# Kernel tuning notes

Hardware: AMD Instinct MI355X
Metric: run time of the kernel (lower is better)

The kernel has to match this reference:

```python
import jax, jax.numpy as jnp
import numpy as np

WS = 8          # window_size
NH = 8          # num_heads
VD = 512        # values_dim
CD = 128        # coords_dim
INNER = 512     # inner_ratio * values_dim
E = INNER // NH # head_dim = 64
B, Hh, Ww_ = 2, 224, 224

# relative position indices (static)
_idx = np.array([[x, y] for x in range(WS) for y in range(WS)])
_rel = _idx[None, :, :] - _idx[:, None, :] + WS - 1  # (WS^2, WS^2, 2)
REL0 = jnp.asarray(_rel[:, :, 0])
REL1 = jnp.asarray(_rel[:, :, 1])

# shifted-window masks (static)
_s = WS * (WS // 2)
_rm = np.zeros((WS * WS, WS * WS), np.float32)
_rm[-_s:, :-_s] = -np.inf
_rm[:-_s, -_s:] = -np.inf
_cm = _rm.reshape(WS, WS, WS, WS).transpose(1, 0, 3, 2).reshape(WS * WS, WS * WS)
ROW_MASK = jnp.asarray(_rm)
COL_MASK = jnp.asarray(_cm)


def _rmsnorm(x, g, eps=1e-6):
    return x * g * jax.lax.rsqrt(jnp.mean(x * x, axis=-1, keepdims=True) + eps)


def _to_windows(x, b, Wh, Ww):
    # x: (b, hp, wp, INNER) with channel layout (e H) (head fastest)
    x = x.reshape(b, Wh, WS, Ww, WS, E, NH)
    return x.transpose(0, 6, 1, 3, 2, 4, 5).reshape(b, NH, Wh, Ww, WS * WS, E)


def setup_inputs() -> dict:
    key = jax.random.key(0)
    ks = jax.random.split(key, 8)
    s = 0.02
    return {
        "embedded_values": jax.random.normal(ks[0], (B, Hh, Ww_, VD), jnp.float32),
        "embedded_coords": jax.random.normal(ks[1], (B, Hh, Ww_, CD), jnp.float32),
        "Wqk_v": jax.random.normal(ks[2], (VD, 2 * INNER), jnp.float32) * s,
        "bqk_v": jnp.zeros((2 * INNER,), jnp.float32),
        "g_v": jnp.ones((2 * INNER,), jnp.float32),
        "Wv": jax.random.normal(ks[3], (VD, INNER), jnp.float32) * s,
        "bv": jnp.zeros((INNER,), jnp.float32),
        "Wqk_c": jax.random.normal(ks[4], (CD, 2 * INNER), jnp.float32) * s,
        "bqk_c": jnp.zeros((2 * INNER,), jnp.float32),
        "g_c": jnp.ones((2 * INNER,), jnp.float32),
        "pos_emb": jax.random.normal(ks[5], (2 * WS - 1, 2 * WS - 1), jnp.float32),
        "Wout": jax.random.normal(ks[6], (INNER, VD), jnp.float32) * s,
        "bout": jnp.zeros((VD,), jnp.float32),
    }


def reference(embedded_values, embedded_coords, Wqk_v, bqk_v, g_v, Wv, bv,
              Wqk_c, bqk_c, g_c, pos_emb, Wout, bout):
    b, h, w, _ = embedded_values.shape
    # projections; torch concat then rearrange '(d k)' k=3 interleaves channels -> reshape (..., INNER, 3)
    vqk = _rmsnorm(embedded_values @ Wqk_v + bqk_v, g_v)          # (b,h,w,2*INNER)
    vval = embedded_values @ Wv + bv                               # (b,h,w,INNER)
    v = jnp.concatenate([vqk, vval], axis=-1).reshape(b, h, w, INNER, 3)
    c = _rmsnorm(embedded_coords @ Wqk_c + bqk_c, g_c).reshape(b, h, w, INNER, 2)

    pad_h = (-h) % WS
    pad_w = (-w) % WS
    v = jnp.pad(v, ((0, 0), (0, pad_h), (0, pad_w), (0, 0), (0, 0)))
    c = jnp.pad(c, ((0, 0), (0, pad_h), (0, pad_w), (0, 0), (0, 0)))
    # shifted=True: roll windows by half window (no inverse roll in original)
    v = jnp.roll(v, (-(WS // 2), -(WS // 2)), axis=(1, 2))
    c = jnp.roll(c, (-(WS // 2), -(WS // 2)), axis=(1, 2))

    hp, wp = h + pad_h, w + pad_w
    Wh, Ww = hp // WS, wp // WS
    qv = _to_windows(v[..., 0], b, Wh, Ww)
    kv = _to_windows(v[..., 1], b, Wh, Ww)
    vv = _to_windows(v[..., 2], b, Wh, Ww)
    qc = _to_windows(c[..., 0], b, Wh, Ww)
    kc = _to_windows(c[..., 1], b, Wh, Ww)

    scale = float(E) ** 0.5
    dots = (jnp.einsum('bhijpe,bhijqe->bhijpq', qv, kv)
            + jnp.einsum('bhijpe,bhijqe->bhijpq', qc, kc)) / scale
    dots = dots + pos_emb[REL0, REL1]
    # shifted-window masks on last window row / column
    dots = dots.at[:, :, -1, :].add(ROW_MASK)
    dots = dots.at[:, :, :, -1].add(COL_MASK)

    attn = jax.nn.softmax(dots, axis=-1)
    y = jnp.einsum('bhijpq,bhijqe->bhijpe', attn, vv)
    # un-window; output channel layout is (H e) (head slow)
    y = y.reshape(b, NH, Wh, Ww, WS, WS, E).transpose(0, 2, 4, 3, 5, 1, 6)
    y = y.reshape(b, hp, wp, INNER)[:, :h, :w, :]
    return y @ Wout + bout
```

## Files before the change

### kernel.cpp

```cpp
#include <hip/hip_runtime.h>


using u16 = unsigned short;
typedef short bf16x8 __attribute__((ext_vector_type(8)));
typedef float f32x4 __attribute__((ext_vector_type(4)));
typedef u16 u16x4 __attribute__((ext_vector_type(4)));
typedef u16 u16x8 __attribute__((ext_vector_type(8)));

__device__ __forceinline__ float bf2f(u16 v) {
  return __uint_as_float(((unsigned)v) << 16);
}
__device__ __forceinline__ u16 f2bf(float f) {
  unsigned u = __float_as_uint(f);
  u += 0x7fffu + ((u >> 16) & 1u);
  return (u16)(u >> 16);
}

__global__ void prep_wv(const float* __restrict__ Wqkv, const float* __restrict__ Wv,
                        u16* __restrict__ out) {
  int idx = blockIdx.x * 256 + threadIdx.x;
  if (idx >= 1536 * 512) return;
  int j = idx >> 9, kk = idx & 511;
  int t = j >> 9, rr = j & 511, nn = rr >> 6, e = rr & 63;
  int cc = 3 * (e * 8 + nn) + t;
  float v = (cc < 1024) ? Wqkv[kk * 1024 + cc] : Wv[kk * 512 + (cc - 1024)];
  out[idx] = f2bf(v);
}

__global__ void prep_wc(const float* __restrict__ W, u16* __restrict__ out) {
  int idx = blockIdx.x * 256 + threadIdx.x;
  if (idx >= 1024 * 128) return;
  int j = idx >> 7, kk = idx & 127;
  int t = j >> 9, rr = j & 511, nn = rr >> 6, e = rr & 63;
  int cc = 2 * (e * 8 + nn) + t;
  out[idx] = f2bf(W[kk * 1024 + cc]);
}

__global__ void prep_wout(const float* __restrict__ W, u16* __restrict__ out) {
  int idx = blockIdx.x * 256 + threadIdx.x;
  if (idx >= 512 * 512) return;
  int o = idx >> 9, kk = idx & 511;
  out[idx] = f2bf(W[kk * 512 + o]);
}

__global__ void prep_vec(const float* __restrict__ bqkv, const float* __restrict__ g_v,
                         const float* __restrict__ bv, const float* __restrict__ bqkc,
                         const float* __restrict__ g_c,
                         float* __restrict__ bpv, float* __restrict__ gAv, float* __restrict__ gBv,
                         float* __restrict__ bpc, float* __restrict__ gAc, float* __restrict__ gBc) {
  int j = blockIdx.x * 256 + threadIdx.x;
  if (j < 1536) {
    int t = j >> 9, rr = j & 511, nn = rr >> 6, e = rr & 63;
    int cc = 3 * (e * 8 + nn) + t;
    if (cc < 1024) { bpv[j] = bqkv[cc]; gAv[j] = g_v[cc]; gBv[j] = 0.f; }
    else           { bpv[j] = bv[cc - 1024]; gAv[j] = 0.f; gBv[j] = 1.f; }
  }
  if (j < 1024) {
    int t = j >> 9, rr = j & 511, nn = rr >> 6, e = rr & 63;
    int cc = 2 * (e * 8 + nn) + t;
    bpc[j] = bqkc[cc]; gAc[j] = g_c[cc]; gBc[j] = 0.f;
  }
}

__global__ void prep_biasT(const float* __restrict__ pe, float* __restrict__ bT) {
  int idx = blockIdx.x * 256 + threadIdx.x;
  if (idx >= 4 * 4096) return;
  int v = idx >> 12, q = (idx >> 6) & 63, p = idx & 63;
  int ap = p >> 3, bp = p & 7, aq = q >> 3, bq = q & 7;
  float val = pe[(aq - ap + 7) * 15 + (bq - bp + 7)];
  if ((v & 1) && ((ap >= 4) != (aq >= 4))) val = -1e30f;
  if ((v & 2) && ((bp >= 4) != (bq >= 4))) val = -1e30f;
  bT[idx] = val;
}

template<bool AFP32>
__device__ __forceinline__ u16x8 load_conv(const void* base, size_t elemoff) {
  if constexpr (AFP32) {
    const float* p = (const float*)base + elemoff;
    float4 lo = *(const float4*)p;
    float4 hi = *(const float4*)(p + 4);
    u16x8 o;
    o[0] = f2bf(lo.x); o[1] = f2bf(lo.y); o[2] = f2bf(lo.z); o[3] = f2bf(lo.w);
    o[4] = f2bf(hi.x); o[5] = f2bf(hi.y); o[6] = f2bf(hi.z); o[7] = f2bf(hi.w);
    return o;
  } else {
    return *(const u16x8*)((const u16*)base + elemoff);
  }
}

template<int N, int K, int MODE, bool AFP32>
__global__ __launch_bounds__(256) void gemm_bt(
    const void* __restrict__ A, const u16* __restrict__ Bt,
    const float* __restrict__ bias, void* __restrict__ outp,
    float* __restrict__ part, const float* __restrict__ gB) {
  constexpr int NCB = N / 128;
  const int bn = blockIdx.x, bm = blockIdx.y;
  const int tid = threadIdx.x;
  const int wid = tid >> 6;
  const int wr = wid >> 1, wc = wid & 1;
  const int lane = tid & 63;
  const int g = lane >> 4, c = lane & 15;
  const int r0 = tid >> 3, ch = tid & 7;

  __shared__ u16 At[128 * 72];
  __shared__ u16 Bs[128 * 72];

  f32x4 acc[4][4] = {};

  const size_t abase = (size_t)bm * 128 * K;
  const u16* Bg = Bt + (size_t)bn * 128 * K;

  u16x8 areg[4], breg[4];
#pragma unroll
  for (int i = 0; i < 4; ++i) {
    int r = i * 32 + r0;
    areg[i] = load_conv<AFP32>(A, abase + (size_t)r * K + ch * 8);
    breg[i] = *(const u16x8*)(Bg + (size_t)r * K + ch * 8);
  }
  constexpr int KT = K / 64;
  for (int kt = 0; kt < KT; ++kt) {
#pragma unroll
    for (int i = 0; i < 4; ++i) {
      int r = i * 32 + r0;
      *(u16x8*)(At + r * 72 + ch * 8) = areg[i];
      *(u16x8*)(Bs + r * 72 + ch * 8) = breg[i];
    }
    __syncthreads();
    if (kt + 1 < KT) {
      const int k0 = (kt + 1) * 64;
#pragma unroll
      for (int i = 0; i < 4; ++i) {
        int r = i * 32 + r0;
        areg[i] = load_conv<AFP32>(A, abase + (size_t)r * K + k0 + ch * 8);
        breg[i] = *(const u16x8*)(Bg + (size_t)r * K + k0 + ch * 8);
      }
    }
#pragma unroll
    for (int kk = 0; kk < 2; ++kk) {
      bf16x8 af[4], bfv[4];
#pragma unroll
      for (int mi = 0; mi < 4; ++mi)
        af[mi] = *(const bf16x8*)(At + (wr * 64 + mi * 16 + c) * 72 + kk * 32 + g * 8);
#pragma unroll
      for (int ni = 0; ni < 4; ++ni)
        bfv[ni] = *(const bf16x8*)(Bs + (wc * 64 + ni * 16 + c) * 72 + kk * 32 + g * 8);
#pragma unroll
      for (int mi = 0; mi < 4; ++mi)
#pragma unroll
        for (int ni = 0; ni < 4; ++ni)
          acc[mi][ni] = __builtin_amdgcn_mfma_f32_16x16x32_bf16(af[mi], bfv[ni], acc[mi][ni], 0, 0, 0);
    }
    __syncthreads();
  }

  const int rowbase = bm * 128 + wr * 64;
  const int colbase = bn * 128 + wc * 64;
  if constexpr (MODE == 0) {
    u16* O = (u16*)outp;
    float rowsq[4][4];
#pragma unroll
    for (int mi = 0; mi < 4; ++mi)
#pragma unroll
      for (int r = 0; r < 4; ++r) rowsq[mi][r] = 0.f;
#pragma unroll
    for (int ni = 0; ni < 4; ++ni) {
      const int col = colbase + ni * 16 + c;
      const float bb = bias[col];
      const float fl = (gB[col] == 0.f) ? 1.f : 0.f;
#pragma unroll
      for (int mi = 0; mi < 4; ++mi)
#pragma unroll
        for (int r = 0; r < 4; ++r) {
          float v = acc[mi][ni][r] + bb;
          O[(size_t)(rowbase + mi * 16 + g * 4 + r) * N + col] = f2bf(v);
          rowsq[mi][r] += fl * v * v;
        }
    }
#pragma unroll
    for (int mi = 0; mi < 4; ++mi)
#pragma unroll
      for (int r = 0; r < 4; ++r) {
        float s = rowsq[mi][r];
        s += __shfl_xor(s, 1); s += __shfl_xor(s, 2);
        s += __shfl_xor(s, 4); s += __shfl_xor(s, 8);
        rowsq[mi][r] = s;
      }
    __syncthreads();
    float* red = (float*)At;
    if (c == 0) {
#pragma unroll
      for (int mi = 0; mi < 4; ++mi)
#pragma unroll
        for (int r = 0; r < 4; ++r)
          red[wc * 128 + wr * 64 + mi * 16 + g * 4 + r] = rowsq[mi][r];
    }
    __syncthreads();
    if (tid < 128)
      part[(size_t)(bm * 128 + tid) * NCB + bn] = red[tid] + red[128 + tid];
  } else {
    float* O = (float*)outp;
#pragma unroll
    for (int ni = 0; ni < 4; ++ni) {
      const int col = colbase + ni * 16 + c;
      const float bb = bias[col];
#pragma unroll
      for (int mi = 0; mi < 4; ++mi)
#pragma unroll
        for (int r = 0; r < 4; ++r)
          O[(size_t)(rowbase + mi * 16 + g * 4 + r) * N + col] = acc[mi][ni][r] + bb;
    }
  }
}

__global__ void combine_scales(const float* __restrict__ pvp, const float* __restrict__ pcp,
                               float* __restrict__ sv, float* __restrict__ sc) {
  const int i = blockIdx.x * 256 + threadIdx.x;
  float s = 0.f;
#pragma unroll
  for (int k = 0; k < 12; ++k) s += pvp[(size_t)i * 12 + k];
  sv[i] = rsqrtf(s * (1.f / 1024.f) + 1e-6f);
  float s2 = 0.f;
#pragma unroll
  for (int k = 0; k < 8; ++k) s2 += pcp[(size_t)i * 8 + k];
  sc[i] = rsqrtf(s2 * (1.f / 1024.f) + 1e-6f);
}

__device__ __forceinline__ void store_norm(u16* dst, u16x8 raw, const float* gA,
                                           const float* gB, float s, int e0) {
  u16x8 o;
#pragma unroll
  for (int j = 0; j < 8; ++j) {
    float fac = gA[e0 + j] * s + gB[e0 + j];
    o[j] = f2bf(bf2f(raw[j]) * fac);
  }
  *(u16x8*)dst = o;
}

__global__ __launch_bounds__(64) void attn_kernel(
    const u16* __restrict__ Pv, const u16* __restrict__ Pc,
    const float* __restrict__ sv, const float* __restrict__ sc,
    const float* __restrict__ gAv, const float* __restrict__ gBv,
    const float* __restrict__ gAc, const float* __restrict__ gBc,
    const float* __restrict__ biasT, u16* __restrict__ Y) {
  const int l = threadIdx.x;
  int bx = blockIdx.x;
  const int wj = bx % 28; bx /= 28;
  const int wi = bx % 28; bx /= 28;
  const int n = bx & 7;
  const int bi = bx >> 3;

  const int g = l >> 4, c = l & 15;
  const int rr0 = l >> 3, rch = l & 7;

  __shared__ u16 Ka[64 * 72];
  __shared__ u16 Qa[64 * 72];
  __shared__ float gf[640];

  gf[l]       = gAv[n * 64 + l];          gf[64 + l]  = gBv[n * 64 + l];
  gf[128 + l] = gAv[512 + n * 64 + l];    gf[192 + l] = gBv[512 + n * 64 + l];
  gf[256 + l] = gAv[1024 + n * 64 + l];   gf[320 + l] = gBv[1024 + n * 64 + l];
  gf[384 + l] = gAc[n * 64 + l];          gf[448 + l] = gBc[n * 64 + l];
  gf[512 + l] = gAc[512 + n * 64 + l];    gf[576 + l] = gBc[512 + n * 64 + l];

  auto pixof = [&](int a, int b2) -> int {
    int y = wi * 8 + a + 4; if (y >= 224) y -= 224;
    int x = wj * 8 + b2 + 4; if (x >= 224) x -= 224;
    return (bi * 224 + y) * 224 + x;
  };

#pragma unroll
  for (int i = 0; i < 8; ++i) {
    const int pix = pixof(i, rr0);
    const float s = sv[pix];
    const u16* src = Pv + (size_t)pix * 1536 + n * 64 + rch * 8;
    u16x8 q = *(const u16x8*)src;
    u16x8 k = *(const u16x8*)(src + 512);
    store_norm(Qa + (i * 8 + rr0) * 72 + rch * 8, q, gf, gf + 64, s, rch * 8);
    store_norm(Ka + (i * 8 + rr0) * 72 + rch * 8, k, gf + 128, gf + 192, s, rch * 8);
  }

  f32x4 acc[4][4] = {};
  auto qk_accum = [&]() {
#pragma unroll
    for (int kk = 0; kk < 2; ++kk) {
      bf16x8 af[4], bq[4];
#pragma unroll
      for (int mi = 0; mi < 4; ++mi)
        af[mi] = *(const bf16x8*)(Ka + (mi * 16 + c) * 72 + kk * 32 + g * 8);
#pragma unroll
      for (int ni = 0; ni < 4; ++ni)
        bq[ni] = *(const bf16x8*)(Qa + (ni * 16 + c) * 72 + kk * 32 + g * 8);
#pragma unroll
      for (int mi = 0; mi < 4; ++mi)
#pragma unroll
        for (int ni = 0; ni < 4; ++ni)
          acc[mi][ni] = __builtin_amdgcn_mfma_f32_16x16x32_bf16(af[mi], bq[ni], acc[mi][ni], 0, 0, 0);
    }
  };
  qk_accum();

#pragma unroll
  for (int i = 0; i < 8; ++i) {
    const int pix = pixof(i, rr0);
    const float s = sc[pix];
    const u16* src = Pc + (size_t)pix * 1024 + n * 64 + rch * 8;
    u16x8 q = *(const u16x8*)src;
    u16x8 k = *(const u16x8*)(src + 512);
    store_norm(Qa + (i * 8 + rr0) * 72 + rch * 8, q, gf + 384, gf + 448, s, rch * 8);
    store_norm(Ka + (i * 8 + rr0) * 72 + rch * 8, k, gf + 512, gf + 576, s, rch * 8);
  }
  qk_accum();

  u16x8 vreg[8]; float vs_[8];
#pragma unroll
  for (int i = 0; i < 8; ++i) {
    const int pix = pixof(i, rr0);
    vs_[i] = sv[pix];
    vreg[i] = *(const u16x8*)(Pv + (size_t)pix * 1536 + 1024 + n * 64 + rch * 8);
  }

  const int variant = ((wi == 27) ? 1 : 0) | ((wj == 27) ? 2 : 0);
  const float* BT = biasT + variant * 4096;
#pragma unroll
  for (int mi = 0; mi < 4; ++mi)
#pragma unroll
    for (int ni = 0; ni < 4; ++ni)
#pragma unroll
      for (int r = 0; r < 4; ++r) {
        const int q = mi * 16 + g * 4 + r;
        const int p = ni * 16 + c;
        acc[mi][ni][r] = acc[mi][ni][r] * 0.125f + BT[q * 64 + p];
      }
  float rinv[4];
#pragma unroll
  for (int ni = 0; ni < 4; ++ni) {
    float m = -3.0e38f;
#pragma unroll
    for (int mi = 0; mi < 4; ++mi)
#pragma unroll
      for (int r = 0; r < 4; ++r) m = fmaxf(m, acc[mi][ni][r]);
    m = fmaxf(m, __shfl_xor(m, 16));
    m = fmaxf(m, __shfl_xor(m, 32));
    float ssum = 0.f;
#pragma unroll
    for (int mi = 0; mi < 4; ++mi)
#pragma unroll
      for (int r = 0; r < 4; ++r) {
        float e = __expf(acc[mi][ni][r] - m);
        acc[mi][ni][r] = e;
        ssum += e;
      }
    ssum += __shfl_xor(ssum, 16);
    ssum += __shfl_xor(ssum, 32);
    rinv[ni] = 1.f / ssum;
  }

  u16* Pl = Qa;
#pragma unroll
  for (int mi = 0; mi < 4; ++mi)
#pragma unroll
    for (int ni = 0; ni < 4; ++ni) {
      u16x4 pk;
#pragma unroll
      for (int r = 0; r < 4; ++r) pk[r] = f2bf(acc[mi][ni][r] * rinv[ni]);
      *(u16x4*)(Pl + (ni * 16 + c) * 72 + mi * 16 + g * 4) = pk;
    }
  u16* Vl = Ka;
#pragma unroll
  for (int i = 0; i < 8; ++i)
    store_norm(Vl + (i * 8 + rr0) * 72 + rch * 8, vreg[i], gf + 256, gf + 320, vs_[i], rch * 8);

  f32x4 ya[4][4] = {};
#pragma unroll
  for (int kk = 0; kk < 2; ++kk) {
    bf16x8 pa[4];
#pragma unroll
    for (int mi = 0; mi < 4; ++mi)
      pa[mi] = *(const bf16x8*)(Pl + (mi * 16 + c) * 72 + kk * 32 + g * 8);
#pragma unroll
    for (int ni = 0; ni < 4; ++ni) {
      u16x8 vtmp;
#pragma unroll
      for (int j = 0; j < 8; ++j)
        vtmp[j] = Vl[(kk * 32 + g * 8 + j) * 72 + ni * 16 + c];
      bf16x8 vb = *(bf16x8*)&vtmp;
#pragma unroll
      for (int mi = 0; mi < 4; ++mi)
        ya[mi][ni] = __builtin_amdgcn_mfma_f32_16x16x32_bf16(pa[mi], vb, ya[mi][ni], 0, 0, 0);
    }
  }

  u16* Yt = Qa;
#pragma unroll
  for (int mi = 0; mi < 4; ++mi)
#pragma unroll
    for (int ni = 0; ni < 4; ++ni) {
      u16x4 yk;
#pragma unroll
      for (int r = 0; r < 4; ++r) yk[r] = f2bf(ya[mi][ni][r]);
      *(u16x4*)(Yt + (ni * 16 + c) * 72 + mi * 16 + g * 4) = yk;
    }
  const int oy = wi * 8 + rr0, ox = wj * 8 + rch;
  u16* dst = Y + ((size_t)(bi * 224 + oy) * 224 + ox) * 512 + n * 64;
#pragma unroll
  for (int chn = 0; chn < 8; ++chn) {
    u16x8 row;
#pragma unroll
    for (int j = 0; j < 8; ++j) row[j] = Yt[(chn * 8 + j) * 72 + l];
    *(u16x8*)(dst + chn * 8) = row;
  }
}

extern "C" void kernel_launch(void* const* d_in, const int* in_sizes, int n_in,
                              void* d_out, int out_size, void* d_ws, size_t ws_size,
                              hipStream_t stream) {
  const float* ev   = (const float*)d_in[0];
  const float* ec   = (const float*)d_in[1];
  const float* Wqkv = (const float*)d_in[2];
  const float* bqkv = (const float*)d_in[3];
  const float* g_v  = (const float*)d_in[4];
  const float* Wv   = (const float*)d_in[5];
  const float* bv   = (const float*)d_in[6];
  const float* Wqkc = (const float*)d_in[7];
  const float* bqkc = (const float*)d_in[8];
  const float* g_c  = (const float*)d_in[9];
  const float* pe   = (const float*)d_in[10];
  const float* Wout = (const float*)d_in[11];
  const float* bout = (const float*)d_in[12];
  float* out = (float*)d_out;

  char* w = (char*)d_ws;
  auto take = [&](size_t b) { char* p = w; w += (b + 255) & ~(size_t)255; return p; };
  u16* Wvp   = (u16*)take(1536ull * 512 * 2);
  u16* Wcp   = (u16*)take(1024ull * 128 * 2);
  u16* Wob   = (u16*)take(512ull * 512 * 2);
  float* bpv = (float*)take(1536 * 4);
  float* gAv = (float*)take(1536 * 4);
  float* gBv = (float*)take(1536 * 4);
  float* bpc = (float*)take(1024 * 4);
  float* gAc = (float*)take(1024 * 4);
  float* gBc = (float*)take(1024 * 4);
  float* bT  = (float*)take(4 * 4096 * 4);
  u16* Pv    = (u16*)take(100352ull * 1536 * 2);
  u16* Pc    = (u16*)take(100352ull * 1024 * 2);
  float* pvp = (float*)take(100352ull * 12 * 4);
  float* pcp = (float*)take(100352ull * 8 * 4);
  float* sv  = (float*)take(100352ull * 4);
  float* sc  = (float*)take(100352ull * 4);
  u16* Yb    = (u16*)take(100352ull * 512 * 2);

  prep_wv<<<3072, 256, 0, stream>>>(Wqkv, Wv, Wvp);
  prep_wc<<<512, 256, 0, stream>>>(Wqkc, Wcp);
  prep_wout<<<1024, 256, 0, stream>>>(Wout, Wob);
  prep_vec<<<6, 256, 0, stream>>>(bqkv, g_v, bv, bqkc, g_c, bpv, gAv, gBv, bpc, gAc, gBc);
  prep_biasT<<<64, 256, 0, stream>>>(pe, bT);

  gemm_bt<1536, 512, 0, true><<<dim3(12, 784), 256, 0, stream>>>(ev, Wvp, bpv, Pv, pvp, gBv);
  gemm_bt<1024, 128, 0, true><<<dim3(8, 784), 256, 0, stream>>>(ec, Wcp, bpc, Pc, pcp, gBc);
  combine_scales<<<392, 256, 0, stream>>>(pvp, pcp, sv, sc);
  attn_kernel<<<12544, 64, 0, stream>>>(Pv, Pc, sv, sc, gAv, gBv, gAc, gBc, bT, Yb);
  gemm_bt<512, 512, 1, false><<<dim3(4, 784), 256, 0, stream>>>(Yb, Wob, bout, out, nullptr, nullptr);
}
```

Baseline: 885.1 us.

## Pre-convert inputs to bf16 and load GEMM tiles directly into LDS

Inputs are converted to bf16 by separate kernels, reusing the Yb buffer for the values input, so every GEMM reads bf16 A operands. The GEMM tile staging now uses global_load_lds straight into unpadded 64-wide LDS tiles instead of a register prefetch with padded stores. This removes the repeated fp32 reads and conversion across the 12 N-blocks and the register round-trip. In exchange it drops the register double-buffering so loads no longer overlap MFMA, and the unpadded layout may cause LDS bank conflicts on fragment reads.

```diff
diff --git a/kernel.cpp b/kernel.cpp
--- a/kernel.cpp
+++ b/kernel.cpp
@@ -14,6 +14,22 @@
   unsigned u = __float_as_uint(f);
   u += 0x7fffu + ((u >> 16) & 1u);
   return (u16)(u >> 16);
+}
+
+__device__ __forceinline__ void gld16(const u16* g, u16* l) {
+  __builtin_amdgcn_global_load_lds(
+      (const __attribute__((address_space(1))) unsigned*)g,
+      (__attribute__((address_space(3))) unsigned*)l, 16, 0, 0);
+}
+
+__global__ void conv_bf16(const float* __restrict__ in, u16* __restrict__ out) {
+  size_t i = ((size_t)blockIdx.x * 256 + threadIdx.x) * 8;
+  float4 a = *(const float4*)(in + i);
+  float4 b = *(const float4*)(in + i + 4);
+  u16x8 o;
+  o[0] = f2bf(a.x); o[1] = f2bf(a.y); o[2] = f2bf(a.z); o[3] = f2bf(a.w);
+  o[4] = f2bf(b.x); o[5] = f2bf(b.y); o[6] = f2bf(b.z); o[7] = f2bf(b.w);
+  *(u16x8*)(out + i) = o;
 }
 
 __global__ void prep_wv(const float* __restrict__ Wqkv, const float* __restrict__ Wv,
@@ -73,77 +89,47 @@
   bT[idx] = val;
 }
 
-template<bool AFP32>
-__device__ __forceinline__ u16x8 load_conv(const void* base, size_t elemoff) {
-  if constexpr (AFP32) {
-    const float* p = (const float*)base + elemoff;
-    float4 lo = *(const float4*)p;
-    float4 hi = *(const float4*)(p + 4);
-    u16x8 o;
-    o[0] = f2bf(lo.x); o[1] = f2bf(lo.y); o[2] = f2bf(lo.z); o[3] = f2bf(lo.w);
-    o[4] = f2bf(hi.x); o[5] = f2bf(hi.y); o[6] = f2bf(hi.z); o[7] = f2bf(hi.w);
-    return o;
-  } else {
-    return *(const u16x8*)((const u16*)base + elemoff);
-  }
-}
-
-template<int N, int K, int MODE, bool AFP32>
+template<int N, int K, int MODE>
 __global__ __launch_bounds__(256) void gemm_bt(
-    const void* __restrict__ A, const u16* __restrict__ Bt,
+    const u16* __restrict__ A, const u16* __restrict__ Bt,
     const float* __restrict__ bias, void* __restrict__ outp,
     float* __restrict__ part, const float* __restrict__ gB) {
   constexpr int NCB = N / 128;
   const int bn = blockIdx.x, bm = blockIdx.y;
   const int tid = threadIdx.x;
-  const int wid = tid >> 6;
-  const int wr = wid >> 1, wc = wid & 1;
+  const int w = tid >> 6;
   const int lane = tid & 63;
+  const int wr = w >> 1, wc = w & 1;
   const int g = lane >> 4, c = lane & 15;
-  const int r0 = tid >> 3, ch = tid & 7;
-
-  __shared__ u16 At[128 * 72];
-  __shared__ u16 Bs[128 * 72];
+
+  __shared__ u16 As[128 * 64];
+  __shared__ u16 Bs[128 * 64];
 
   f32x4 acc[4][4] = {};
-
-  const size_t abase = (size_t)bm * 128 * K;
+  const u16* Ag = A + (size_t)bm * 128 * K;
   const u16* Bg = Bt + (size_t)bn * 128 * K;
 
-  u16x8 areg[4], breg[4];
-#pragma unroll
-  for (int i = 0; i < 4; ++i) {
-    int r = i * 32 + r0;
-    areg[i] = load_conv<AFP32>(A, abase + (size_t)r * K + ch * 8);
-    breg[i] = *(const u16x8*)(Bg + (size_t)r * K + ch * 8);
-  }
-  constexpr int KT = K / 64;
-  for (int kt = 0; kt < KT; ++kt) {
+  const int lr = lane >> 3;
+  const int lc = (lane & 7) * 8;
+
+  for (int kt = 0; kt < K / 64; ++kt) {
+    const int k0 = kt * 64;
 #pragma unroll
     for (int i = 0; i < 4; ++i) {
-      int r = i * 32 + r0;
-      *(u16x8*)(At + r * 72 + ch * 8) = areg[i];
-      *(u16x8*)(Bs + r * 72 + ch * 8) = breg[i];
+      const int rbase = (w * 4 + i) * 8;
+      gld16(Ag + (size_t)(rbase + lr) * K + k0 + lc, As + rbase * 64 + lane * 8);
+      gld16(Bg + (size_t)(rbase + lr) * K + k0 + lc, Bs + rbase * 64 + lane * 8);
     }
     __syncthreads();
-    if (kt + 1 < KT) {
-      const int k0 = (kt + 1) * 64;
-#pragma unroll
-      for (int i = 0; i < 4; ++i) {
-        int r = i * 32 + r0;
-        areg[i] = load_conv<AFP32>(A, abase + (size_t)r * K + k0 + ch * 8);
-        breg[i] = *(const u16x8*)(Bg + (size_t)r * K + k0 + ch * 8);
-      }
-    }
 #pragma unroll
     for (int kk = 0; kk < 2; ++kk) {
       bf16x8 af[4], bfv[4];
 #pragma unroll
       for (int mi = 0; mi < 4; ++mi)
-        af[mi] = *(const bf16x8*)(At + (wr * 64 + mi * 16 + c) * 72 + kk * 32 + g * 8);
+        af[mi] = *(const bf16x8*)(As + (wr * 64 + mi * 16 + c) * 64 + kk * 32 + g * 8);
 #pragma unroll
       for (int ni = 0; ni < 4; ++ni)
-        bfv[ni] = *(const bf16x8*)(Bs + (wc * 64 + ni * 16 + c) * 72 + kk * 32 + g * 8);
+        bfv[ni] = *(const bf16x8*)(Bs + (wc * 64 + ni * 16 + c) * 64 + kk * 32 + g * 8);
 #pragma unroll
       for (int mi = 0; mi < 4; ++mi)
 #pragma unroll
@@ -186,7 +172,7 @@
         rowsq[mi][r] = s;
       }
     __syncthreads();
-    float* red = (float*)At;
+    float* red = (float*)As;
     if (c == 0) {
 #pragma unroll
       for (int mi = 0; mi < 4; ++mi)
@@ -448,16 +434,20 @@
   float* sv  = (float*)take(100352ull * 4);
   float* sc  = (float*)take(100352ull * 4);
   u16* Yb    = (u16*)take(100352ull * 512 * 2);
-
+  u16* evb   = Yb;
+  u16* ecb   = (u16*)take(100352ull * 128 * 2);
+
+  conv_bf16<<<25088, 256, 0, stream>>>(ev, evb);
+  conv_bf16<<<6272, 256, 0, stream>>>(ec, ecb);
   prep_wv<<<3072, 256, 0, stream>>>(Wqkv, Wv, Wvp);
   prep_wc<<<512, 256, 0, stream>>>(Wqkc, Wcp);
   prep_wout<<<1024, 256, 0, stream>>>(Wout, Wob);
   prep_vec<<<6, 256, 0, stream>>>(bqkv, g_v, bv, bqkc, g_c, bpv, gAv, gBv, bpc, gAc, gBc);
   prep_biasT<<<64, 256, 0, stream>>>(pe, bT);
 
-  gemm_bt<1536, 512, 0, true><<<dim3(12, 784), 256, 0, stream>>>(ev, Wvp, bpv, Pv, pvp, gBv);
-  gemm_bt<1024, 128, 0, true><<<dim3(8, 784), 256, 0, stream>>>(ec, Wcp, bpc, Pc, pcp, gBc);
+  gemm_bt<1536, 512, 0><<<dim3(12, 784), 256, 0, stream>>>(evb, Wvp, bpv, Pv, pvp, gBv);
+  gemm_bt<1024, 128, 0><<<dim3(8, 784), 256, 0, stream>>>(ecb, Wcp, bpc, Pc, pcp, gBc);
   combine_scales<<<392, 256, 0, stream>>>(pvp, pcp, sv, sc);
   attn_kernel<<<12544, 64, 0, stream>>>(Pv, Pc, sv, sc, gAv, gBv, gAc, gBc, bT, Yb);
-  gemm_bt<512, 512, 1, false><<<dim3(4, 784), 256, 0, stream>>>(Yb, Wob, bout, out, nullptr, nullptr);
-}
+  gemm_bt<512, 512, 1><<<dim3(4, 784), 256, 0, stream>>>(Yb, Wob, bout, out, nullptr, nullptr);
+}
```

Measured after the change: 852.7 us. 1.04x faster.
